# Kernel optimization log

Measured on AMD Instinct MI355X. Metric: run time of the kernel, lower is better.

Reference implementation:

```python
import jax, jax.numpy as jnp
import numpy as np
from jax import lax

B, N = 16, 4096


def _fps(xyz, npoint):
    # xyz: [N,3] -> [npoint] int32 indices (iterative farthest point sampling, start at idx 0)
    n = xyz.shape[0]
    def step(carry, _):
        dist, far = carry
        d = jnp.sum((xyz - xyz[far]) ** 2, axis=-1)
        dist = jnp.minimum(dist, d)
        nxt = jnp.argmax(dist).astype(jnp.int32)
        return (dist, nxt), far
    (_, _), idx = lax.scan(step, (jnp.full((n,), 1e10, xyz.dtype), jnp.int32(0)), None, length=npoint)
    return idx


def _ball_query(xyz, new_xyz, radius, nsample):
    # xyz: [N,3], new_xyz: [S,3] -> [S, nsample] neighbor indices within radius
    n = xyz.shape[0]
    sqr = jnp.sum((new_xyz[:, None, :] - xyz[None, :, :]) ** 2, axis=-1)  # [S,N]
    idx = jnp.where(sqr > radius * radius, n, jnp.arange(n)[None, :])
    idx = jnp.sort(idx, axis=-1)[:, :nsample]
    return jnp.where(idx == n, idx[:, :1], idx)  # pad misses with first hit


def _gather(p, i):
    return p[i]


def _mlp(feat, ws):
    # feat: [B,S,K,C]; 1x1 conv + folded eval-BN + ReLU per layer
    for W, b in ws:
        feat = jax.nn.relu(jnp.einsum('bskc,oc->bsko', feat, W) + b)
    return feat


def _sa(xyz, points, npoint, radius, nsample, ws):
    fps_idx = jax.vmap(_fps, in_axes=(0, None))(xyz, npoint)              # [B,S]
    new_xyz = jnp.take_along_axis(xyz, fps_idx[..., None], axis=1)         # [B,S,3]
    idx = jax.vmap(_ball_query, in_axes=(0, 0, None, None))(xyz, new_xyz, radius, nsample)  # [B,S,K]
    grouped_xyz = jax.vmap(_gather)(xyz, idx) - new_xyz[:, :, None, :]     # [B,S,K,3]
    if points is None:
        feat = grouped_xyz
    else:
        feat = jnp.concatenate([grouped_xyz, jax.vmap(_gather)(points, idx)], axis=-1)
    return new_xyz, jnp.max(_mlp(feat, ws), axis=2)                        # [B,S,Cout]


def _forward(x, ws1, ws2, ws3, fw, fb):
    b = x.shape[0]
    l1_xyz, l1_pts = _sa(x, None, 512, 0.2, 32, ws1)       # [B,512,3], [B,512,128]
    l2_xyz, l2_pts = _sa(l1_xyz, l1_pts, 128, 0.4, 64, ws2)  # [B,128,3], [B,128,256]
    feat = jnp.concatenate([l2_xyz, l2_pts], axis=-1)[:, None]  # group_all: [B,1,128,259]
    g = jnp.max(_mlp(feat, ws3), axis=2).reshape(b, 1024)
    return g @ fw.T + fb


_SPECS = [
    ('sa1_w0', (64, 3)), ('sa1_b0', (64,)), ('sa1_w1', (64, 64)), ('sa1_b1', (64,)), ('sa1_w2', (128, 64)), ('sa1_b2', (128,)),
    ('sa2_w0', (128, 131)), ('sa2_b0', (128,)), ('sa2_w1', (128, 128)), ('sa2_b1', (128,)), ('sa2_w2', (256, 128)), ('sa2_b2', (256,)),
    ('sa3_w0', (256, 259)), ('sa3_b0', (256,)), ('sa3_w1', (512, 256)), ('sa3_b1', (512,)), ('sa3_w2', (1024, 512)), ('sa3_b2', (1024,)),
    ('fw', (1024, 1024)), ('fb', (1024,)),
]


def setup_inputs() -> dict:
    key = jax.random.key(0)
    keys = jax.random.split(key, len(_SPECS) + 1)
    inp = {'x': jax.random.uniform(keys[0], (B, N, 3), dtype=jnp.float32)}
    for (name, shp), k in zip(_SPECS, keys[1:]):
        inp[name] = jax.random.normal(k, shp, dtype=jnp.float32) * 0.02
    return inp


def reference(x, sa1_w0, sa1_b0, sa1_w1, sa1_b1, sa1_w2, sa1_b2,
              sa2_w0, sa2_b0, sa2_w1, sa2_b1, sa2_w2, sa2_b2,
              sa3_w0, sa3_b0, sa3_w1, sa3_b1, sa3_w2, sa3_b2, fw, fb):
    ws1 = [(sa1_w0, sa1_b0), (sa1_w1, sa1_b1), (sa1_w2, sa1_b2)]
    ws2 = [(sa2_w0, sa2_b0), (sa2_w1, sa2_b1), (sa2_w2, sa2_b2)]
    ws3 = [(sa3_w0, sa3_b0), (sa3_w1, sa3_b1), (sa3_w2, sa3_b2)]
    return _forward(x, ws1, ws2, ws3, fw, fb)
```

## Files before the change

kernel.cpp:

```cpp
#include <hip/hip_runtime.h>

#ifndef BATCH
#define BATCH 16
#endif

template<int CTRL>
__device__ __forceinline__ float dppmaxf(float v)
{
    const int d = __builtin_amdgcn_update_dpp(__float_as_int(v), __float_as_int(v),
                                              CTRL, 0xf, 0xf, false);
    return fmaxf(v, __int_as_float(d));
}
template<int CTRL>
__device__ __forceinline__ unsigned dppminu(unsigned v)
{
    const unsigned d = (unsigned)__builtin_amdgcn_update_dpp((int)v, (int)v,
                                                             CTRL, 0xf, 0xf, false);
    return (d < v) ? d : v;
}
__device__ __forceinline__ float wave_max_bcast(float v)
{
    v = dppmaxf<0x111>(v);
    v = dppmaxf<0x112>(v);
    v = dppmaxf<0x114>(v);
    v = dppmaxf<0x118>(v);
    v = dppmaxf<0x142>(v);
    v = dppmaxf<0x143>(v);
    return __int_as_float(__builtin_amdgcn_readlane(__float_as_int(v), 63));
}
__device__ __forceinline__ unsigned wave_min_bcast(unsigned v)
{
    v = dppminu<0x111>(v);
    v = dppminu<0x112>(v);
    v = dppminu<0x114>(v);
    v = dppminu<0x118>(v);
    v = dppminu<0x142>(v);
    v = dppminu<0x143>(v);
    return (unsigned)__builtin_amdgcn_readlane((int)v, 63);
}

template<int N, int NP1, int NP2, int BLOCK>
__global__ __launch_bounds__(BLOCK)
void fps_fused(const float* __restrict__ xyz,
               float* __restrict__ out1, float* __restrict__ out2)
{
#pragma clang fp contract(off)
    constexpr int P  = N / BLOCK;
    constexpr int P2 = NP1 / BLOCK;
    __shared__ float sx[N], sy[N], sz[N];
    __shared__ float s2x[NP1], s2y[NP1], s2z[NP1];
    __shared__ float o2x[NP2], o2y[NP2], o2z[NP2];
    __shared__ unsigned long long slot[3];
    const int b = blockIdx.x, t = threadIdx.x;
    const float* xb = xyz + (size_t)b * N * 3;
    float px[P], py[P], pz[P], dist[P];
#pragma unroll
    for (int j = 0; j < P; ++j) {
        const int i = t + j * BLOCK;
        const float x = xb[i*3+0], y = xb[i*3+1], z = xb[i*3+2];
        sx[i] = x; sy[i] = y; sz[i] = z;
        px[j] = x; py[j] = y; pz[j] = z;
        dist[j] = 1e10f;
    }
    if (t < 3) slot[t] = 0ull;
    __syncthreads();
    float fx = sx[0], fy = sy[0], fz = sz[0];
    if (t == 0) { s2x[0] = fx; s2y[0] = fy; s2z[0] = fz; }
    int cur = 1;
    for (int s = 1; s < NP1; ++s) {
        float bestv = -1.f; int besti = 0;
#pragma unroll
        for (int j = 0; j < P; ++j) {
            const float dx = px[j]-fx, dy = py[j]-fy, dz = pz[j]-fz;
            const float d = (dx*dx + dy*dy) + dz*dz;
            const float nd = fminf(dist[j], d);
            dist[j] = nd;
            if (nd > bestv) { bestv = nd; besti = t + j * BLOCK; }
        }
        const float wm = wave_max_bcast(bestv);
        const unsigned cand = (bestv == wm) ? (unsigned)besti : 0xffffffffu;
        const unsigned wi = wave_min_bcast(cand);
        if ((t & 63) == 0) {
            const unsigned long long pk =
                ((unsigned long long)__float_as_uint(wm) << 32) | (unsigned)(~wi);
            atomicMax(&slot[cur], pk);
        }
        const int nxt = (cur == 2) ? 0 : cur + 1;
        if (t == 0) slot[nxt] = 0ull;
        __syncthreads();
        const int far = (int)(~(unsigned)slot[cur]);
        fx = sx[far]; fy = sy[far]; fz = sz[far];
        if (t == 0) { s2x[s] = fx; s2y[s] = fy; s2z[s] = fz; }
        cur = nxt;
    }
    __syncthreads();
    if (t < 3) slot[t] = 0ull;
    __syncthreads();
    float mx[P2], my[P2], mz[P2], d2[P2];
#pragma unroll
    for (int j = 0; j < P2; ++j) {
        const int i = t + j * BLOCK;
        mx[j] = s2x[i]; my[j] = s2y[i]; mz[j] = s2z[i];
        d2[j] = 1e10f;
    }
    fx = s2x[0]; fy = s2y[0]; fz = s2z[0];
    if (t == 0) { o2x[0] = fx; o2y[0] = fy; o2z[0] = fz; }
    cur = 1;
    for (int s = 1; s < NP2; ++s) {
        float bestv = -1.f; int besti = 0;
#pragma unroll
        for (int j = 0; j < P2; ++j) {
            const float dx = mx[j]-fx, dy = my[j]-fy, dz = mz[j]-fz;
            const float d = (dx*dx + dy*dy) + dz*dz;
            const float nd = fminf(d2[j], d);
            d2[j] = nd;
            if (nd > bestv) { bestv = nd; besti = t + j * BLOCK; }
        }
        const float wm = wave_max_bcast(bestv);
        const unsigned cand = (bestv == wm) ? (unsigned)besti : 0xffffffffu;
        const unsigned wi = wave_min_bcast(cand);
        if ((t & 63) == 0) {
            const unsigned long long pk =
                ((unsigned long long)__float_as_uint(wm) << 32) | (unsigned)(~wi);
            atomicMax(&slot[cur], pk);
        }
        const int nxt = (cur == 2) ? 0 : cur + 1;
        if (t == 0) slot[nxt] = 0ull;
        __syncthreads();
        const int far2 = (int)(~(unsigned)slot[cur]);
        fx = s2x[far2]; fy = s2y[far2]; fz = s2z[far2];
        if (t == 0) { o2x[s] = fx; o2y[s] = fy; o2z[s] = fz; }
        cur = nxt;
    }
    __syncthreads();
    for (int i = t; i < NP1; i += BLOCK) {
        out1[((size_t)b*NP1 + i)*3 + 0] = s2x[i];
        out1[((size_t)b*NP1 + i)*3 + 1] = s2y[i];
        out1[((size_t)b*NP1 + i)*3 + 2] = s2z[i];
    }
    for (int i = t; i < NP2; i += BLOCK) {
        out2[((size_t)b*NP2 + i)*3 + 0] = o2x[i];
        out2[((size_t)b*NP2 + i)*3 + 1] = o2y[i];
        out2[((size_t)b*NP2 + i)*3 + 2] = o2z[i];
    }
}

template<int N, int S, int K>
__global__ __launch_bounds__(256)
void ballq_kernel(const float* __restrict__ xyz, const float* __restrict__ nxyz,
                  int* __restrict__ idx, const float r2)
{
#pragma clang fp contract(off)
    const int gw = (blockIdx.x * 256 + threadIdx.x) >> 6;
    const int lane = threadIdx.x & 63;
    const int b = gw / S, s = gw % S;
    const float* xb = xyz + (size_t)b * N * 3;
    const float qx = nxyz[((size_t)b*S + s)*3 + 0];
    const float qy = nxyz[((size_t)b*S + s)*3 + 1];
    const float qz = nxyz[((size_t)b*S + s)*3 + 2];
    int* op = idx + ((size_t)b*S + s) * K;
    int base = 0, first = -1;
    for (int c = 0; c < N; c += 64) {
        const int i = c + lane;
        const float dx = xb[i*3+0]-qx, dy = xb[i*3+1]-qy, dz = xb[i*3+2]-qz;
        const float d = (dx*dx + dy*dy) + dz*dz;
        const bool hit = !(d > r2);
        const unsigned long long m = __ballot(hit);
        if (first < 0 && m) first = c + __builtin_ctzll(m);
        const int pos = base + __popcll(m & ((1ull << lane) - 1ull));
        if (hit && pos < K) op[pos] = i;
        base += __popcll(m);
        if (base >= K) break;
    }
    if (base < K && lane >= base && lane < K) op[lane] = first;
}

__global__ __launch_bounds__(256)
void transpose_all(const float* __restrict__ s0, float* __restrict__ d0,
                   const float* __restrict__ s1, float* __restrict__ d1,
                   const float* __restrict__ s2, float* __restrict__ d2,
                   const float* __restrict__ s3, float* __restrict__ d3,
                   const float* __restrict__ s4, float* __restrict__ d4,
                   const float* __restrict__ s5, float* __restrict__ d5,
                   const float* __restrict__ s6, float* __restrict__ d6,
                   const float* __restrict__ s7, float* __restrict__ d7,
                   const float* __restrict__ s8, float* __restrict__ d8)
{
    int i = blockIdx.x * 256 + threadIdx.x;
    if (i < 192)    { d0[(i%3)  *64   + i/3  ] = s0[i]; return; }  i -= 192;
    if (i < 4096)   { d1[(i&63) *64   + (i>>6)] = s1[i]; return; } i -= 4096;
    if (i < 8192)   { d2[(i&63) *128  + (i>>6)] = s2[i]; return; } i -= 8192;
    if (i < 16768)  { d3[(i%131)*128  + i/131] = s3[i]; return; }  i -= 16768;
    if (i < 16384)  { d4[(i&127)*128  + (i>>7)] = s4[i]; return; } i -= 16384;
    if (i < 32768)  { d5[(i&127)*256  + (i>>7)] = s5[i]; return; } i -= 32768;
    if (i < 66304)  { d6[(i%259)*256  + i/259] = s6[i]; return; }  i -= 66304;
    if (i < 131072) { d7[(i&255)*512  + (i>>8)] = s7[i]; return; } i -= 131072;
    if (i < 524288) { d8[(i&511)*1024 + (i>>9)] = s8[i]; return; }
}

__device__ __forceinline__ void fma16(float (&acc)[16], const float f,
                                      const float* __restrict__ wrow)
{
    const float4 w0 = ((const float4*)wrow)[0];
    const float4 w1 = ((const float4*)wrow)[1];
    const float4 w2 = ((const float4*)wrow)[2];
    const float4 w3 = ((const float4*)wrow)[3];
    acc[0]+=f*w0.x;  acc[1]+=f*w0.y;  acc[2]+=f*w0.z;  acc[3]+=f*w0.w;
    acc[4]+=f*w1.x;  acc[5]+=f*w1.y;  acc[6]+=f*w1.z;  acc[7]+=f*w1.w;
    acc[8]+=f*w2.x;  acc[9]+=f*w2.y;  acc[10]+=f*w2.z; acc[11]+=f*w2.w;
    acc[12]+=f*w3.x; acc[13]+=f*w3.y; acc[14]+=f*w3.z; acc[15]+=f*w3.w;
}

__global__ __launch_bounds__(256)
void sa1_fused(const float* __restrict__ xyz, const float* __restrict__ nxyz,
               const int* __restrict__ idx,
               const float* __restrict__ Wt0, const float* __restrict__ B0,
               const float* __restrict__ Wt1, const float* __restrict__ B1,
               const float* __restrict__ Wt2, const float* __restrict__ B2,
               float* __restrict__ out)
{
    __shared__ float buf[64][64];
    const int tid = threadIdx.x, lane = tid & 63;
    const int wave = __builtin_amdgcn_readfirstlane(tid >> 6);
    const int row0 = blockIdx.x * 64;
    const int myrow = row0 + lane;
    const int g = myrow >> 5, b = g >> 9;
    const int i = idx[myrow];
    const float* p = xyz + ((size_t)b*4096 + i) * 3;
    const float f0 = p[0] - nxyz[(size_t)g*3 + 0];
    const float f1 = p[1] - nxyz[(size_t)g*3 + 1];
    const float f2 = p[2] - nxyz[(size_t)g*3 + 2];
    const int oc0 = wave * 16;
    float aL[16], aH[16];
#pragma unroll
    for (int j = 0; j < 16; ++j)
        aL[j] = B0[oc0+j] + f0*Wt0[0*64+oc0+j] + f1*Wt0[1*64+oc0+j] + f2*Wt0[2*64+oc0+j];
#pragma unroll
    for (int j = 0; j < 16; ++j) buf[oc0+j][lane] = fmaxf(aL[j], 0.f);
    __syncthreads();
#pragma unroll
    for (int j = 0; j < 16; ++j) aL[j] = B1[oc0+j];
#pragma unroll 4
    for (int ci = 0; ci < 64; ++ci)
        fma16(aL, buf[ci][lane], Wt1 + ci*64 + oc0);
    __syncthreads();
#pragma unroll
    for (int j = 0; j < 16; ++j) buf[oc0+j][lane] = fmaxf(aL[j], 0.f);
    __syncthreads();
#pragma unroll
    for (int j = 0; j < 16; ++j) { aL[j] = B2[oc0+j]; aH[j] = B2[64+oc0+j]; }
#pragma unroll 2
    for (int ci = 0; ci < 64; ++ci) {
        const float f = buf[ci][lane];
        fma16(aL, f, Wt2 + ci*128 + oc0);
        fma16(aH, f, Wt2 + ci*128 + 64 + oc0);
    }
#pragma unroll
    for (int j = 0; j < 16; ++j) {
        float v = fmaxf(aL[j], 0.f);
        v = fmaxf(v, __shfl_xor(v, 1));
        v = fmaxf(v, __shfl_xor(v, 2));
        v = fmaxf(v, __shfl_xor(v, 4));
        v = fmaxf(v, __shfl_xor(v, 8));
        v = fmaxf(v, __shfl_xor(v, 16));
        float w = fmaxf(aH[j], 0.f);
        w = fmaxf(w, __shfl_xor(w, 1));
        w = fmaxf(w, __shfl_xor(w, 2));
        w = fmaxf(w, __shfl_xor(w, 4));
        w = fmaxf(w, __shfl_xor(w, 8));
        w = fmaxf(w, __shfl_xor(w, 16));
        if ((lane & 31) == 0) {
            const size_t orow = (size_t)((row0 + lane) >> 5) * 128;
            out[orow + oc0 + j] = v;
            out[orow + 64 + oc0 + j] = w;
        }
    }
}

__global__ __launch_bounds__(256)
void sa2_fused(const float* __restrict__ l1xyz, const float* __restrict__ l1pts,
               const float* __restrict__ nxyz, const int* __restrict__ idx,
               const float* __restrict__ Wt0, const float* __restrict__ B0,
               const float* __restrict__ Wt1, const float* __restrict__ B1,
               const float* __restrict__ Wt2, const float* __restrict__ B2,
               float* __restrict__ out)
{
    __shared__ float buf[128][64];
    const int tid = threadIdx.x, lane = tid & 63;
    const int wave = __builtin_amdgcn_readfirstlane(tid >> 6);
    const int gblk = blockIdx.x;
    const int b = gblk >> 7;
    const int row0 = gblk * 64;
    const int myi = idx[row0 + lane];
    const float* pc = l1xyz + ((size_t)b*512 + myi) * 3;
    const float f0 = pc[0] - nxyz[(size_t)gblk*3 + 0];
    const float f1 = pc[1] - nxyz[(size_t)gblk*3 + 1];
    const float f2 = pc[2] - nxyz[(size_t)gblk*3 + 2];
    for (int r = wave; r < 64; r += 4) {
        const int i2 = idx[row0 + r];
        const float* src = l1pts + ((size_t)b*512 + i2) * 128;
        buf[lane][r ^ lane]    = src[lane];
        buf[lane+64][r ^ lane] = src[lane + 64];
    }
    __syncthreads();
    const int oc0 = wave * 16;
    float aL[16], aH[16];
#pragma unroll
    for (int j = 0; j < 16; ++j) {
        aL[j] = B0[oc0+j]    + f0*Wt0[0*128+oc0+j]    + f1*Wt0[1*128+oc0+j]    + f2*Wt0[2*128+oc0+j];
        aH[j] = B0[64+oc0+j] + f0*Wt0[0*128+64+oc0+j] + f1*Wt0[1*128+64+oc0+j] + f2*Wt0[2*128+64+oc0+j];
    }
#pragma unroll 2
    for (int ci = 0; ci < 128; ++ci) {
        const float f = buf[ci][lane ^ (ci & 63)];
        const float* wp = Wt0 + (size_t)(ci+3)*128;
        fma16(aL, f, wp + oc0);
        fma16(aH, f, wp + 64 + oc0);
    }
    __syncthreads();
#pragma unroll
    for (int j = 0; j < 16; ++j) {
        buf[oc0+j][lane]    = fmaxf(aL[j], 0.f);
        buf[64+oc0+j][lane] = fmaxf(aH[j], 0.f);
    }
    __syncthreads();
#pragma unroll
    for (int j = 0; j < 16; ++j) { aL[j] = B1[oc0+j]; aH[j] = B1[64+oc0+j]; }
#pragma unroll 2
    for (int ci = 0; ci < 128; ++ci) {
        const float f = buf[ci][lane];
        const float* wp = Wt1 + (size_t)ci*128;
        fma16(aL, f, wp + oc0);
        fma16(aH, f, wp + 64 + oc0);
    }
    __syncthreads();
#pragma unroll
    for (int j = 0; j < 16; ++j) {
        buf[oc0+j][lane]    = fmaxf(aL[j], 0.f);
        buf[64+oc0+j][lane] = fmaxf(aH[j], 0.f);
    }
    __syncthreads();
    float* orow = out + (size_t)gblk * 256;
    for (int half = 0; half < 2; ++half) {
        const int oc = half*128 + oc0;
#pragma unroll
        for (int j = 0; j < 16; ++j) { aL[j] = B2[oc+j]; aH[j] = B2[64+oc+j]; }
#pragma unroll 2
        for (int ci = 0; ci < 128; ++ci) {
            const float f = buf[ci][lane];
            const float* wp = Wt2 + (size_t)ci*256;
            fma16(aL, f, wp + oc);
            fma16(aH, f, wp + 64 + oc);
        }
#pragma unroll
        for (int j = 0; j < 16; ++j) {
            float v = fmaxf(aL[j], 0.f);
            v = fmaxf(v, __shfl_xor(v, 1));
            v = fmaxf(v, __shfl_xor(v, 2));
            v = fmaxf(v, __shfl_xor(v, 4));
            v = fmaxf(v, __shfl_xor(v, 8));
            v = fmaxf(v, __shfl_xor(v, 16));
            v = fmaxf(v, __shfl_xor(v, 32));
            float w = fmaxf(aH[j], 0.f);
            w = fmaxf(w, __shfl_xor(w, 1));
            w = fmaxf(w, __shfl_xor(w, 2));
            w = fmaxf(w, __shfl_xor(w, 4));
            w = fmaxf(w, __shfl_xor(w, 8));
            w = fmaxf(w, __shfl_xor(w, 16));
            w = fmaxf(w, __shfl_xor(w, 32));
            if (lane == 0) { orow[oc + j] = v; orow[64 + oc + j] = w; }
        }
    }
}

template<int CIN, int COUT, bool CONCAT3, bool POOL>
__global__ __launch_bounds__(256)
void mlp_gemm_kernel(const float* __restrict__ inA, const float* __restrict__ inB,
                     const float* __restrict__ Wt, const float* __restrict__ Bb,
                     float* __restrict__ out)
{
    __shared__ float featS[128][64];
    const int tid = threadIdx.x, lane = tid & 63;
    const int wave = __builtin_amdgcn_readfirstlane(tid >> 6);
    const int row0 = blockIdx.x * 64;
    const int oc0 = blockIdx.y * 64 + wave * 16;
    float acc[16];
#pragma unroll
    for (int j = 0; j < 16; ++j) acc[j] = Bb[oc0 + j];
    for (int c0 = 0; c0 < CIN; c0 += 128) {
        const int csz = (CIN - c0 < 128) ? (CIN - c0) : 128;
        __syncthreads();
        for (int r = wave; r < 64; r += 4) {
            const int row = row0 + r;
            for (int cl = lane; cl < csz; cl += 64) {
                const int cig = c0 + cl;
                float v;
                if (CONCAT3)
                    v = (cig < 3) ? inA[(size_t)row*3 + cig]
                                  : inB[(size_t)row*(CIN-3) + (cig - 3)];
                else
                    v = inA[(size_t)row*CIN + cig];
                featS[cl][r ^ (cl & 63)] = v;
            }
        }
        __syncthreads();
        if (csz == 128) {
#pragma unroll 4
            for (int ci = 0; ci < 128; ++ci)
                fma16(acc, featS[ci][lane ^ (ci & 63)], Wt + (size_t)(c0+ci)*COUT + oc0);
        } else {
            for (int ci = 0; ci < csz; ++ci)
                fma16(acc, featS[ci][lane ^ (ci & 63)], Wt + (size_t)(c0+ci)*COUT + oc0);
        }
    }
    if (POOL) {
#pragma unroll
        for (int j = 0; j < 16; ++j) {
            float v = fmaxf(acc[j], 0.f);
            v = fmaxf(v, __shfl_xor(v, 1));
            v = fmaxf(v, __shfl_xor(v, 2));
            v = fmaxf(v, __shfl_xor(v, 4));
            v = fmaxf(v, __shfl_xor(v, 8));
            v = fmaxf(v, __shfl_xor(v, 16));
            v = fmaxf(v, __shfl_xor(v, 32));
            if (lane == 0) out[(size_t)blockIdx.x * COUT + oc0 + j] = v;
        }
    } else {
        float4 o0, o1, o2, o3;
        o0.x=fmaxf(acc[0],0.f);  o0.y=fmaxf(acc[1],0.f);  o0.z=fmaxf(acc[2],0.f);  o0.w=fmaxf(acc[3],0.f);
        o1.x=fmaxf(acc[4],0.f);  o1.y=fmaxf(acc[5],0.f);  o1.z=fmaxf(acc[6],0.f);  o1.w=fmaxf(acc[7],0.f);
        o2.x=fmaxf(acc[8],0.f);  o2.y=fmaxf(acc[9],0.f);  o2.z=fmaxf(acc[10],0.f); o2.w=fmaxf(acc[11],0.f);
        o3.x=fmaxf(acc[12],0.f); o3.y=fmaxf(acc[13],0.f); o3.z=fmaxf(acc[14],0.f); o3.w=fmaxf(acc[15],0.f);
        float4* op = (float4*)(out + (size_t)(row0 + lane)*COUT + oc0);
        op[0]=o0; op[1]=o1; op[2]=o2; op[3]=o3;
    }
}

__global__ __launch_bounds__(256)
void fc_kernel(const float* __restrict__ pmax, const float* __restrict__ fw,
               const float* __restrict__ fb, float* __restrict__ y)
{
    const int gw = (blockIdx.x * 256 + threadIdx.x) >> 6;
    const int lane = threadIdx.x & 63;
    const int b = gw >> 10, o = gw & 1023;
    const float4* g0 = (const float4*)(pmax + (size_t)(2*b) * 1024);
    const float4* g1 = (const float4*)(pmax + (size_t)(2*b+1) * 1024);
    const float4* wv = (const float4*)(fw + (size_t)o * 1024);
    float acc = 0.f;
#pragma unroll
    for (int r = 0; r < 4; ++r) {
        const float4 a = g0[lane + r*64];
        const float4 c = g1[lane + r*64];
        const float4 w = wv[lane + r*64];
        acc += fmaxf(a.x,c.x)*w.x + fmaxf(a.y,c.y)*w.y
             + fmaxf(a.z,c.z)*w.z + fmaxf(a.w,c.w)*w.w;
    }
#pragma unroll
    for (int m = 32; m >= 1; m >>= 1) acc += __shfl_xor(acc, m);
    if (lane == 0) y[gw] = acc + fb[o];
}

extern "C" void kernel_launch(void* const* d_in, const int* in_sizes, int n_in,
                              void* d_out, int out_size, void* d_ws, size_t ws_size,
                              hipStream_t stream)
{
    (void)in_sizes; (void)n_in; (void)out_size; (void)ws_size;
    const float* x   = (const float*)d_in[0];
    const float* s1w0 = (const float*)d_in[1];  const float* s1b0 = (const float*)d_in[2];
    const float* s1w1 = (const float*)d_in[3];  const float* s1b1 = (const float*)d_in[4];
    const float* s1w2 = (const float*)d_in[5];  const float* s1b2 = (const float*)d_in[6];
    const float* s2w0 = (const float*)d_in[7];  const float* s2b0 = (const float*)d_in[8];
    const float* s2w1 = (const float*)d_in[9];  const float* s2b1 = (const float*)d_in[10];
    const float* s2w2 = (const float*)d_in[11]; const float* s2b2 = (const float*)d_in[12];
    const float* s3w0 = (const float*)d_in[13]; const float* s3b0 = (const float*)d_in[14];
    const float* s3w1 = (const float*)d_in[15]; const float* s3b1 = (const float*)d_in[16];
    const float* s3w2 = (const float*)d_in[17]; const float* s3b2 = (const float*)d_in[18];
    const float* fw  = (const float*)d_in[19]; const float* fb  = (const float*)d_in[20];
    float* y = (float*)d_out;

    char* ws = (char*)d_ws;
    float* l1_xyz = (float*)(ws + 0);
    int*   idx1   = (int*)  (ws + 98304);
    float* l1_pts = (float*)(ws + 1146880);
    float* l2_xyz = (float*)(ws + 5341184);
    int*   idx2   = (int*)  (ws + 5365760);
    float* l2_pts = (float*)(ws + 5890048);
    float* h1     = (float*)(ws + 7987200);
    float* h2     = (float*)(ws + 10084352);
    float* pmax   = (float*)(ws + 14278656);
    float* wt1_0  = (float*)(ws + 14409728);
    float* wt1_1  = (float*)(ws + 14410496);
    float* wt1_2  = (float*)(ws + 14426880);
    float* wt2_0  = (float*)(ws + 14459648);
    float* wt2_1  = (float*)(ws + 14526720);
    float* wt2_2  = (float*)(ws + 14592256);
    float* wt3_0  = (float*)(ws + 14723328);
    float* wt3_1  = (float*)(ws + 14988544);
    float* wt3_2  = (float*)(ws + 15512832);

    const float r2_1 = (float)(0.2 * 0.2);
    const float r2_2 = (float)(0.4 * 0.4);

    transpose_all<<<3126, 256, 0, stream>>>(
        s1w0, wt1_0, s1w1, wt1_1, s1w2, wt1_2,
        s2w0, wt2_0, s2w1, wt2_1, s2w2, wt2_2,
        s3w0, wt3_0, s3w1, wt3_1, s3w2, wt3_2);

    fps_fused<4096, 512, 128, 256><<<BATCH, 256, 0, stream>>>(x, l1_xyz, l2_xyz);
    ballq_kernel<4096, 512, 32><<<(BATCH*512)/4, 256, 0, stream>>>(x, l1_xyz, idx1, r2_1);
    sa1_fused<<<(BATCH*512*32)/64, 256, 0, stream>>>(x, l1_xyz, idx1,
        wt1_0, s1b0, wt1_1, s1b1, wt1_2, s1b2, l1_pts);
    ballq_kernel<512, 128, 64><<<(BATCH*128)/4, 256, 0, stream>>>(l1_xyz, l2_xyz, idx2, r2_2);
    sa2_fused<<<BATCH*128, 256, 0, stream>>>(l1_xyz, l1_pts, l2_xyz, idx2,
        wt2_0, s2b0, wt2_1, s2b1, wt2_2, s2b2, l2_pts);
    mlp_gemm_kernel<259, 256,  true,  false><<<dim3(32, 4),  256, 0, stream>>>(l2_xyz, l2_pts, wt3_0, s3b0, h1);
    mlp_gemm_kernel<256, 512,  false, false><<<dim3(32, 8),  256, 0, stream>>>(h1, nullptr, wt3_1, s3b1, h2);
    mlp_gemm_kernel<512, 1024, false, true ><<<dim3(32, 16), 256, 0, stream>>>(h2, nullptr, wt3_2, s3b2, pmax);
    fc_kernel<<<(BATCH*1024)/4, 256, 0, stream>>>(pmax, fw, fb, y);
}
```

Before: 948.0 us.

## Replace FPS LDS atomics with per-wave slots, merge ball queries, pack FMAs

Farthest-point sampling now writes each wave's packed max/index to a double-buffered per-wave shared slot and has every thread reduce the slots after the barrier. This replaces the LDS 64-bit atomicMax and the rotating slot reset. Both ball-query launches are merged into one kernel, which saves a launch. The MLP kernels accumulate in two-wide float vectors so the compiler can emit packed fp32 FMA instructions. The packed arithmetic may change contraction and register pressure.

```diff
diff --git a/kernel.cpp b/kernel.cpp
--- a/kernel.cpp
+++ b/kernel.cpp
@@ -3,6 +3,9 @@
 #ifndef BATCH
 #define BATCH 16
 #endif
+
+typedef float f32x2 __attribute__((ext_vector_type(2)));
+__device__ __forceinline__ f32x2 mk2(float a, float b) { f32x2 r; r.x = a; r.y = b; return r; }
 
 template<int CTRL>
 __device__ __forceinline__ float dppmaxf(float v)
@@ -47,11 +50,13 @@
 #pragma clang fp contract(off)
     constexpr int P  = N / BLOCK;
     constexpr int P2 = NP1 / BLOCK;
+    constexpr int NW = BLOCK / 64;
     __shared__ float sx[N], sy[N], sz[N];
     __shared__ float s2x[NP1], s2y[NP1], s2z[NP1];
     __shared__ float o2x[NP2], o2y[NP2], o2z[NP2];
-    __shared__ unsigned long long slot[3];
+    __shared__ unsigned long long wslot[2][NW];
     const int b = blockIdx.x, t = threadIdx.x;
+    const int lane = t & 63, wv = t >> 6;
     const float* xb = xyz + (size_t)b * N * 3;
     float px[P], py[P], pz[P], dist[P];
 #pragma unroll
@@ -62,11 +67,9 @@
         px[j] = x; py[j] = y; pz[j] = z;
         dist[j] = 1e10f;
     }
-    if (t < 3) slot[t] = 0ull;
     __syncthreads();
     float fx = sx[0], fy = sy[0], fz = sz[0];
     if (t == 0) { s2x[0] = fx; s2y[0] = fy; s2z[0] = fz; }
-    int cur = 1;
     for (int s = 1; s < NP1; ++s) {
         float bestv = -1.f; int besti = 0;
 #pragma unroll
@@ -80,21 +83,21 @@
         const float wm = wave_max_bcast(bestv);
         const unsigned cand = (bestv == wm) ? (unsigned)besti : 0xffffffffu;
         const unsigned wi = wave_min_bcast(cand);
-        if ((t & 63) == 0) {
-            const unsigned long long pk =
-                ((unsigned long long)__float_as_uint(wm) << 32) | (unsigned)(~wi);
-            atomicMax(&slot[cur], pk);
-        }
-        const int nxt = (cur == 2) ? 0 : cur + 1;
-        if (t == 0) slot[nxt] = 0ull;
+        const int par = s & 1;
+        if (lane == 0)
+            wslot[par][wv] = ((unsigned long long)__float_as_uint(wm) << 32)
+                           | (unsigned)(~wi);
         __syncthreads();
-        const int far = (int)(~(unsigned)slot[cur]);
+        unsigned long long pa = wslot[par][0];
+#pragma unroll
+        for (int w = 1; w < NW; ++w) {
+            const unsigned long long pb = wslot[par][w];
+            pa = (pb > pa) ? pb : pa;
+        }
+        const int far = (int)(~(unsigned)pa);
         fx = sx[far]; fy = sy[far]; fz = sz[far];
         if (t == 0) { s2x[s] = fx; s2y[s] = fy; s2z[s] = fz; }
-        cur = nxt;
-    }
-    __syncthreads();
-    if (t < 3) slot[t] = 0ull;
+    }
     __syncthreads();
     float mx[P2], my[P2], mz[P2], d2[P2];
 #pragma unroll
@@ -105,7 +108,6 @@
     }
     fx = s2x[0]; fy = s2y[0]; fz = s2z[0];
     if (t == 0) { o2x[0] = fx; o2y[0] = fy; o2z[0] = fz; }
-    cur = 1;
     for (int s = 1; s < NP2; ++s) {
         float bestv = -1.f; int besti = 0;
 #pragma unroll
@@ -119,18 +121,20 @@
         const float wm = wave_max_bcast(bestv);
         const unsigned cand = (bestv == wm) ? (unsigned)besti : 0xffffffffu;
         const unsigned wi = wave_min_bcast(cand);
-        if ((t & 63) == 0) {
-            const unsigned long long pk =
-                ((unsigned long long)__float_as_uint(wm) << 32) | (unsigned)(~wi);
-            atomicMax(&slot[cur], pk);
-        }
-        const int nxt = (cur == 2) ? 0 : cur + 1;
-        if (t == 0) slot[nxt] = 0ull;
+        const int par = s & 1;
+        if (lane == 0)
+            wslot[par][wv] = ((unsigned long long)__float_as_uint(wm) << 32)
+                           | (unsigned)(~wi);
         __syncthreads();
-        const int far2 = (int)(~(unsigned)slot[cur]);
+        unsigned long long pa = wslot[par][0];
+#pragma unroll
+        for (int w = 1; w < NW; ++w) {
+            const unsigned long long pb = wslot[par][w];
+            pa = (pb > pa) ? pb : pa;
+        }
+        const int far2 = (int)(~(unsigned)pa);
         fx = s2x[far2]; fy = s2y[far2]; fz = s2z[far2];
         if (t == 0) { o2x[s] = fx; o2y[s] = fy; o2z[s] = fz; }
-        cur = nxt;
     }
     __syncthreads();
     for (int i = t; i < NP1; i += BLOCK) {
@@ -146,13 +150,14 @@
 }
 
 template<int N, int S, int K>
-__global__ __launch_bounds__(256)
-void ballq_kernel(const float* __restrict__ xyz, const float* __restrict__ nxyz,
-                  int* __restrict__ idx, const float r2)
+__device__ __forceinline__ void ballq_body(const float* __restrict__ xyz,
+                                           const float* __restrict__ nxyz,
+                                           int* __restrict__ idx, const float r2,
+                                           const int bid, const int tid)
 {
 #pragma clang fp contract(off)
-    const int gw = (blockIdx.x * 256 + threadIdx.x) >> 6;
-    const int lane = threadIdx.x & 63;
+    const int gw = (bid * 256 + tid) >> 6;
+    const int lane = tid & 63;
     const int b = gw / S, s = gw % S;
     const float* xb = xyz + (size_t)b * N * 3;
     const float qx = nxyz[((size_t)b*S + s)*3 + 0];
@@ -176,6 +181,19 @@
 }
 
 __global__ __launch_bounds__(256)
+void ballq_both(const float* __restrict__ pts1, const float* __restrict__ q1,
+                int* __restrict__ idx1, const float r2a,
+                const float* __restrict__ pts2, const float* __restrict__ q2,
+                int* __restrict__ idx2, const float r2b)
+{
+    const int nb1 = (BATCH * 512) / 4;
+    if ((int)blockIdx.x < nb1)
+        ballq_body<4096, 512, 32>(pts1, q1, idx1, r2a, blockIdx.x, threadIdx.x);
+    else
+        ballq_body<512, 128, 64>(pts2, q2, idx2, r2b, blockIdx.x - nb1, threadIdx.x);
+}
+
+__global__ __launch_bounds__(256)
 void transpose_all(const float* __restrict__ s0, float* __restrict__ d0,
                    const float* __restrict__ s1, float* __restrict__ d1,
                    const float* __restrict__ s2, float* __restrict__ d2,
@@ -198,17 +216,37 @@
     if (i < 524288) { d8[(i&511)*1024 + (i>>9)] = s8[i]; return; }
 }
 
-__device__ __forceinline__ void fma16(float (&acc)[16], const float f,
-                                      const float* __restrict__ wrow)
+__device__ __forceinline__ void fma16pk(f32x2 (&acc)[8], const float f,
+                                        const float* __restrict__ wrow)
 {
     const float4 w0 = ((const float4*)wrow)[0];
     const float4 w1 = ((const float4*)wrow)[1];
     const float4 w2 = ((const float4*)wrow)[2];
     const float4 w3 = ((const float4*)wrow)[3];
-    acc[0]+=f*w0.x;  acc[1]+=f*w0.y;  acc[2]+=f*w0.z;  acc[3]+=f*w0.w;
-    acc[4]+=f*w1.x;  acc[5]+=f*w1.y;  acc[6]+=f*w1.z;  acc[7]+=f*w1.w;
-    acc[8]+=f*w2.x;  acc[9]+=f*w2.y;  acc[10]+=f*w2.z; acc[11]+=f*w2.w;
-    acc[12]+=f*w3.x; acc[13]+=f*w3.y; acc[14]+=f*w3.z; acc[15]+=f*w3.w;
+    const f32x2 ff = mk2(f, f);
+    acc[0] += ff * mk2(w0.x, w0.y);
+    acc[1] += ff * mk2(w0.z, w0.w);
+    acc[2] += ff * mk2(w1.x, w1.y);
+    acc[3] += ff * mk2(w1.z, w1.w);
+    acc[4] += ff * mk2(w2.x, w2.y);
+    acc[5] += ff * mk2(w2.z, w2.w);
+    acc[6] += ff * mk2(w3.x, w3.y);
+    acc[7] += ff * mk2(w3.z, w3.w);
+}
+
+__device__ __forceinline__ float pool_half(float v)
+{
+    v = fmaxf(v, __shfl_xor(v, 1));
+    v = fmaxf(v, __shfl_xor(v, 2));
+    v = fmaxf(v, __shfl_xor(v, 4));
+    v = fmaxf(v, __shfl_xor(v, 8));
+    v = fmaxf(v, __shfl_xor(v, 16));
+    return v;
+}
+__device__ __forceinline__ float pool_full(float v)
+{
+    v = pool_half(v);
+    return fmaxf(v, __shfl_xor(v, 32));
 }
 
 __global__ __launch_bounds__(256)
@@ -231,48 +269,48 @@
     const float f1 = p[1] - nxyz[(size_t)g*3 + 1];
     const float f2 = p[2] - nxyz[(size_t)g*3 + 2];
     const int oc0 = wave * 16;
-    float aL[16], aH[16];
-#pragma unroll
-    for (int j = 0; j < 16; ++j)
-        aL[j] = B0[oc0+j] + f0*Wt0[0*64+oc0+j] + f1*Wt0[1*64+oc0+j] + f2*Wt0[2*64+oc0+j];
-#pragma unroll
-    for (int j = 0; j < 16; ++j) buf[oc0+j][lane] = fmaxf(aL[j], 0.f);
-    __syncthreads();
-#pragma unroll
-    for (int j = 0; j < 16; ++j) aL[j] = B1[oc0+j];
+    f32x2 aL[8], aH[8];
+#pragma unroll
+    for (int j = 0; j < 16; ++j) {
+        const float v = B0[oc0+j] + f0*Wt0[0*64+oc0+j] + f1*Wt0[1*64+oc0+j] + f2*Wt0[2*64+oc0+j];
+        buf[oc0+j][lane] = fmaxf(v, 0.f);
+    }
+    __syncthreads();
+#pragma unroll
+    for (int k = 0; k < 8; ++k) aL[k] = mk2(B1[oc0+2*k], B1[oc0+2*k+1]);
 #pragma unroll 4
     for (int ci = 0; ci < 64; ++ci)
-        fma16(aL, buf[ci][lane], Wt1 + ci*64 + oc0);
-    __syncthreads();
-#pragma unroll
-    for (int j = 0; j < 16; ++j) buf[oc0+j][lane] = fmaxf(aL[j], 0.f);
-    __syncthreads();
-#pragma unroll
-    for (int j = 0; j < 16; ++j) { aL[j] = B2[oc0+j]; aH[j] = B2[64+oc0+j]; }
+        fma16pk(aL, buf[ci][lane], Wt1 + ci*64 + oc0);
+    __syncthreads();
+#pragma unroll
+    for (int k = 0; k < 8; ++k) {
+        buf[oc0+2*k][lane]   = fmaxf(aL[k].x, 0.f);
+        buf[oc0+2*k+1][lane] = fmaxf(aL[k].y, 0.f);
+    }
+    __syncthreads();
+#pragma unroll
+    for (int k = 0; k < 8; ++k) {
+        aL[k] = mk2(B2[oc0+2*k], B2[oc0+2*k+1]);
+        aH[k] = mk2(B2[64+oc0+2*k], B2[64+oc0+2*k+1]);
+    }
 #pragma unroll 2
     for (int ci = 0; ci < 64; ++ci) {
         const float f = buf[ci][lane];
-        fma16(aL, f, Wt2 + ci*128 + oc0);
-        fma16(aH, f, Wt2 + ci*128 + 64 + oc0);
-    }
-#pragma unroll
-    for (int j = 0; j < 16; ++j) {
-        float v = fmaxf(aL[j], 0.f);
-        v = fmaxf(v, __shfl_xor(v, 1));
-        v = fmaxf(v, __shfl_xor(v, 2));
-        v = fmaxf(v, __shfl_xor(v, 4));
-        v = fmaxf(v, __shfl_xor(v, 8));
-        v = fmaxf(v, __shfl_xor(v, 16));
-        float w = fmaxf(aH[j], 0.f);
-        w = fmaxf(w, __shfl_xor(w, 1));
-        w = fmaxf(w, __shfl_xor(w, 2));
-        w = fmaxf(w, __shfl_xor(w, 4));
-        w = fmaxf(w, __shfl_xor(w, 8));
-        w = fmaxf(w, __shfl_xor(w, 16));
+        fma16pk(aL, f, Wt2 + ci*128 + oc0);
+        fma16pk(aH, f, Wt2 + ci*128 + 64 + oc0);
+    }
+#pragma unroll
+    for (int k = 0; k < 8; ++k) {
+        const float v0 = pool_half(fmaxf(aL[k].x, 0.f));
+        const float v1 = pool_half(fmaxf(aL[k].y, 0.f));
+        const float w0 = pool_half(fmaxf(aH[k].x, 0.f));
+        const float w1 = pool_half(fmaxf(aH[k].y, 0.f));
         if ((lane & 31) == 0) {
             const size_t orow = (size_t)((row0 + lane) >> 5) * 128;
-            out[orow + oc0 + j] = v;
-            out[orow + 64 + oc0 + j] = w;
+            out[orow + oc0 + 2*k]       = v0;
+            out[orow + oc0 + 2*k + 1]   = v1;
+            out[orow + 64 + oc0 + 2*k]     = w0;
+            out[orow + 64 + oc0 + 2*k + 1] = w1;
         }
     }
 }
@@ -304,71 +342,79 @@
     }
     __syncthreads();
     const int oc0 = wave * 16;
-    float aL[16], aH[16];
-#pragma unroll
-    for (int j = 0; j < 16; ++j) {
-        aL[j] = B0[oc0+j]    + f0*Wt0[0*128+oc0+j]    + f1*Wt0[1*128+oc0+j]    + f2*Wt0[2*128+oc0+j];
-        aH[j] = B0[64+oc0+j] + f0*Wt0[0*128+64+oc0+j] + f1*Wt0[1*128+64+oc0+j] + f2*Wt0[2*128+64+oc0+j];
+    f32x2 aL[8], aH[8];
+#pragma unroll
+    for (int k = 0; k < 8; ++k) {
+        const int j0 = oc0 + 2*k, j1 = oc0 + 2*k + 1;
+        aL[k] = mk2(B0[j0]    + f0*Wt0[j0]     + f1*Wt0[128+j0]    + f2*Wt0[256+j0],
+                    B0[j1]    + f0*Wt0[j1]     + f1*Wt0[128+j1]    + f2*Wt0[256+j1]);
+        aH[k] = mk2(B0[64+j0] + f0*Wt0[64+j0]  + f1*Wt0[192+j0]    + f2*Wt0[320+j0],
+                    B0[64+j1] + f0*Wt0[64+j1]  + f1*Wt0[192+j1]    + f2*Wt0[320+j1]);
     }
 #pragma unroll 2
     for (int ci = 0; ci < 128; ++ci) {
         const float f = buf[ci][lane ^ (ci & 63)];
         const float* wp = Wt0 + (size_t)(ci+3)*128;
-        fma16(aL, f, wp + oc0);
-        fma16(aH, f, wp + 64 + oc0);
-    }
-    __syncthreads();
-#pragma unroll
-    for (int j = 0; j < 16; ++j) {
-        buf[oc0+j][lane]    = fmaxf(aL[j], 0.f);
-        buf[64+oc0+j][lane] = fmaxf(aH[j], 0.f);
-    }
-    __syncthreads();
-#pragma unroll
-    for (int j = 0; j < 16; ++j) { aL[j] = B1[oc0+j]; aH[j] = B1[64+oc0+j]; }
+        fma16pk(aL, f, wp + oc0);
+        fma16pk(aH, f, wp + 64 + oc0);
+    }
+    __syncthreads();
+#pragma unroll
+    for (int k = 0; k < 8; ++k) {
+        buf[oc0+2*k][lane]      = fmaxf(aL[k].x, 0.f);
+        buf[oc0+2*k+1][lane]    = fmaxf(aL[k].y, 0.f);
+        buf[64+oc0+2*k][lane]   = fmaxf(aH[k].x, 0.f);
+        buf[64+oc0+2*k+1][lane] = fmaxf(aH[k].y, 0.f);
+    }
+    __syncthreads();
+#pragma unroll
+    for (int k = 0; k < 8; ++k) {
+        aL[k] = mk2(B1[oc0+2*k], B1[oc0+2*k+1]);
+        aH[k] = mk2(B1[64+oc0+2*k], B1[64+oc0+2*k+1]);
+    }
 #pragma unroll 2
     for (int ci = 0; ci < 128; ++ci) {
         const float f = buf[ci][lane];
         const float* wp = Wt1 + (size_t)ci*128;
-        fma16(aL, f, wp + oc0);
-        fma16(aH, f, wp + 64 + oc0);
-    }
-    __syncthreads();
-#pragma unroll
-    for (int j = 0; j < 16; ++j) {
-        buf[oc0+j][lane]    = fmaxf(aL[j], 0.f);
-        buf[64+oc0+j][lane] = fmaxf(aH[j], 0.f);
+        fma16pk(aL, f, wp + oc0);
+        fma16pk(aH, f, wp + 64 + oc0);
+    }
+    __syncthreads();
+#pragma unroll
+    for (int k = 0; k < 8; ++k) {
+        buf[oc0+2*k][lane]      = fmaxf(aL[k].x, 0.f);
+        buf[oc0+2*k+1][lane]    = fmaxf(aL[k].y, 0.f);
+        buf[64+oc0+2*k][lane]   = fmaxf(aH[k].x, 0.f);
+        buf[64+oc0+2*k+1][lane] = fmaxf(aH[k].y, 0.f);
     }
     __syncthreads();
     float* orow = out + (size_t)gblk * 256;
     for (int half = 0; half < 2; ++half) {
         const int oc = half*128 + oc0;
 #pragma unroll
-        for (int j = 0; j < 16; ++j) { aL[j] = B2[oc+j]; aH[j] = B2[64+oc+j]; }
+        for (int k = 0; k < 8; ++k) {
+            aL[k] = mk2(B2[oc+2*k], B2[oc+2*k+1]);
+            aH[k] = mk2(B2[64+oc+2*k], B2[64+oc+2*k+1]);
+        }
 #pragma unroll 2
         for (int ci = 0; ci < 128; ++ci) {
             const float f = buf[ci][lane];
             const float* wp = Wt2 + (size_t)ci*256;
-            fma16(aL, f, wp + oc);
-            fma16(aH, f, wp + 64 + oc);
-        }
-#pragma unroll
-        for (int j = 0; j < 16; ++j) {
-            float v = fmaxf(aL[j], 0.f);
-            v = fmaxf(v, __shfl_xor(v, 1));
-            v = fmaxf(v, __shfl_xor(v, 2));
-            v = fmaxf(v, __shfl_xor(v, 4));
-            v = fmaxf(v, __shfl_xor(v, 8));
-            v = fmaxf(v, __shfl_xor(v, 16));
-            v = fmaxf(v, __shfl_xor(v, 32));
-            float w = fmaxf(aH[j], 0.f);
-            w = fmaxf(w, __shfl_xor(w, 1));
-            w = fmaxf(w, __shfl_xor(w, 2));
-            w = fmaxf(w, __shfl_xor(w, 4));
-            w = fmaxf(w, __shfl_xor(w, 8));
-            w = fmaxf(w, __shfl_xor(w, 16));
-            w = fmaxf(w, __shfl_xor(w, 32));
-            if (lane == 0) { orow[oc + j] = v; orow[64 + oc + j] = w; }
+            fma16pk(aL, f, wp + oc);
+            fma16pk(aH, f, wp + 64 + oc);
+        }
+#pragma unroll
+        for (int k = 0; k < 8; ++k) {
+            const float v0 = pool_full(fmaxf(aL[k].x, 0.f));
+            const float v1 = pool_full(fmaxf(aL[k].y, 0.f));
+            const float w0 = pool_full(fmaxf(aH[k].x, 0.f));
+            const float w1 = pool_full(fmaxf(aH[k].y, 0.f));
+            if (lane == 0) {
+                orow[oc + 2*k]        = v0;
+                orow[oc + 2*k + 1]    = v1;
+                orow[64 + oc + 2*k]   = w0;
+                orow[64 + oc + 2*k+1] = w1;
+            }
         }
     }
 }
@@ -384,9 +430,9 @@
     const int wave = __builtin_amdgcn_readfirstlane(tid >> 6);
     const int row0 = blockIdx.x * 64;
     const int oc0 = blockIdx.y * 64 + wave * 16;
-    float acc[16];
-#pragma unroll
-    for (int j = 0; j < 16; ++j) acc[j] = Bb[oc0 + j];
+    f32x2 acc[8];
+#pragma unroll
+    for (int k = 0; k < 8; ++k) acc[k] = mk2(Bb[oc0+2*k], Bb[oc0+2*k+1]);
     for (int c0 = 0; c0 < CIN; c0 += 128) {
         const int csz = (CIN - c0 < 128) ? (CIN - c0) : 128;
         __syncthreads();
@@ -407,30 +453,28 @@
         if (csz == 128) {
 #pragma unroll 4
             for (int ci = 0; ci < 128; ++ci)
-                fma16(acc, featS[ci][lane ^ (ci & 63)], Wt + (size_t)(c0+ci)*COUT + oc0);
+                fma16pk(acc, featS[ci][lane ^ (ci & 63)], Wt + (size_t)(c0+ci)*COUT + oc0);
         } else {
             for (int ci = 0; ci < csz; ++ci)
-                fma16(acc, featS[ci][lane ^ (ci & 63)], Wt + (size_t)(c0+ci)*COUT + oc0);
+                fma16pk(acc, featS[ci][lane ^ (ci & 63)], Wt + (size_t)(c0+ci)*COUT + oc0);
         }
     }
     if (POOL) {
 #pragma unroll
-        for (int j = 0; j < 16; ++j) {
-            float v = fmaxf(acc[j], 0.f);
-            v = fmaxf(v, __shfl_xor(v, 1));
-            v = fmaxf(v, __shfl_xor(v, 2));
-            v = fmaxf(v, __shfl_xor(v, 4));
-            v = fmaxf(v, __shfl_xor(v, 8));
-            v = fmaxf(v, __shfl_xor(v, 16));
-            v = fmaxf(v, __shfl_xor(v, 32));
-            if (lane == 0) out[(size_t)blockIdx.x * COUT + oc0 + j] = v;
+        for (int k = 0; k < 8; ++k) {
+            const float v0 = pool_full(fmaxf(acc[k].x, 0.f));
+            const float v1 = pool_full(fmaxf(acc[k].y, 0.f));
+            if (lane == 0) {
+                out[(size_t)blockIdx.x * COUT + oc0 + 2*k]     = v0;
+                out[(size_t)blockIdx.x * COUT + oc0 + 2*k + 1] = v1;
+            }
         }
     } else {
         float4 o0, o1, o2, o3;
-        o0.x=fmaxf(acc[0],0.f);  o0.y=fmaxf(acc[1],0.f);  o0.z=fmaxf(acc[2],0.f);  o0.w=fmaxf(acc[3],0.f);
-        o1.x=fmaxf(acc[4],0.f);  o1.y=fmaxf(acc[5],0.f);  o1.z=fmaxf(acc[6],0.f);  o1.w=fmaxf(acc[7],0.f);
-        o2.x=fmaxf(acc[8],0.f);  o2.y=fmaxf(acc[9],0.f);  o2.z=fmaxf(acc[10],0.f); o2.w=fmaxf(acc[11],0.f);
-        o3.x=fmaxf(acc[12],0.f); o3.y=fmaxf(acc[13],0.f); o3.z=fmaxf(acc[14],0.f); o3.w=fmaxf(acc[15],0.f);
+        o0.x=fmaxf(acc[0].x,0.f); o0.y=fmaxf(acc[0].y,0.f); o0.z=fmaxf(acc[1].x,0.f); o0.w=fmaxf(acc[1].y,0.f);
+        o1.x=fmaxf(acc[2].x,0.f); o1.y=fmaxf(acc[2].y,0.f); o1.z=fmaxf(acc[3].x,0.f); o1.w=fmaxf(acc[3].y,0.f);
+        o2.x=fmaxf(acc[4].x,0.f); o2.y=fmaxf(acc[4].y,0.f); o2.z=fmaxf(acc[5].x,0.f); o2.w=fmaxf(acc[5].y,0.f);
+        o3.x=fmaxf(acc[6].x,0.f); o3.y=fmaxf(acc[6].y,0.f); o3.z=fmaxf(acc[7].x,0.f); o3.w=fmaxf(acc[7].y,0.f);
         float4* op = (float4*)(out + (size_t)(row0 + lane)*COUT + oc0);
         op[0]=o0; op[1]=o1; op[2]=o2; op[3]=o3;
     }
@@ -507,10 +551,10 @@
         s3w0, wt3_0, s3w1, wt3_1, s3w2, wt3_2);
 
     fps_fused<4096, 512, 128, 256><<<BATCH, 256, 0, stream>>>(x, l1_xyz, l2_xyz);
-    ballq_kernel<4096, 512, 32><<<(BATCH*512)/4, 256, 0, stream>>>(x, l1_xyz, idx1, r2_1);
+    ballq_both<<<(BATCH*512)/4 + (BATCH*128)/4, 256, 0, stream>>>(
+        x, l1_xyz, idx1, r2_1, l1_xyz, l2_xyz, idx2, r2_2);
     sa1_fused<<<(BATCH*512*32)/64, 256, 0, stream>>>(x, l1_xyz, idx1,
         wt1_0, s1b0, wt1_1, s1b1, wt1_2, s1b2, l1_pts);
-    ballq_kernel<512, 128, 64><<<(BATCH*128)/4, 256, 0, stream>>>(l1_xyz, l2_xyz, idx2, r2_2);
     sa2_fused<<<BATCH*128, 256, 0, stream>>>(l1_xyz, l1_pts, l2_xyz, idx2,
         wt2_0, s2b0, wt2_1, s2b1, wt2_2, s2b2, l2_pts);
     mlp_gemm_kernel<259, 256,  true,  false><<<dim3(32, 4),  256, 0, stream>>>(l2_xyz, l2_pts, wt3_0, s3b0, h1);
```

Result: no change. 939.5 us (-0.9%).
